# Optimization experiments

Hardware: AMD Instinct MI355X
Metric: run time of the kernel (lower is better)

The kernel has to match this reference:

```python
import jax, jax.numpy as jnp
import numpy as np

N = 100000      # nodes
E = 1_600_000   # edges (avg degree 16)
DIMS = [(64, 64), (64, 64), (64, 40)]  # gnn_layers [64,64,64,40]


def setup_inputs() -> dict:
    key = jax.random.key(0)
    ks = jax.random.split(key, 2 + 3 * len(DIMS))
    inp = {
        "x": jax.random.normal(ks[0], (N, DIMS[0][0]), jnp.float32),
        "edge_index": jax.random.randint(ks[1], (2, E), 0, N),
    }
    k = 2
    for i, (din, dout) in enumerate(DIMS):
        s = 1.0 / np.sqrt(din)
        inp[f"Wl{i}"] = jax.random.uniform(ks[k], (din, dout), jnp.float32, -s, s); k += 1
        inp[f"bl{i}"] = jax.random.uniform(ks[k], (dout,), jnp.float32, -s, s); k += 1
        inp[f"Wr{i}"] = jax.random.uniform(ks[k], (din, dout), jnp.float32, -s, s); k += 1
    return inp


def _sage_conv(x, src, dst, Wl, bl, Wr):
    # PyG SAGEConv (mean aggr): out = lin_l(mean_{j in N(i)} x_j) + lin_r(x_i)
    deg = jax.ops.segment_sum(jnp.ones((src.shape[0],), x.dtype), dst, num_segments=N)
    agg = jax.ops.segment_sum(x[src], dst, num_segments=N)  # [N, din] scatter-add
    agg = agg / jnp.clip(deg, 1.0)[:, None]                  # mean; isolated nodes -> 0
    return agg @ Wl + bl + x @ Wr


def reference(x, edge_index, Wl0, bl0, Wr0, Wl1, bl1, Wr1, Wl2, bl2, Wr2):
    src, dst = edge_index[0], edge_index[1]
    h = x
    params = [(Wl0, bl0, Wr0), (Wl1, bl1, Wr1), (Wl2, bl2, Wr2)]
    for i, (Wl, bl, Wr) in enumerate(params):
        h = _sage_conv(h, src, dst, Wl, bl, Wr)
        if i != len(params) - 1:
            h = jax.nn.relu(h)
            # F.dropout with training=False is identity (eval mode)
    return jax.nn.log_softmax(h, axis=1)
```

## Files before the change

### kernel.cpp

```cpp
#include <hip/hip_runtime.h>
#include <math.h>

#define ACT_RELU 0
#define ACT_LSM  1
#define BSH 8
#define MAXNB 512

typedef __attribute__((ext_vector_type(8))) short bf16x8;
typedef __attribute__((ext_vector_type(4))) float f32x4;

__device__ __forceinline__ unsigned f2bf(float f) {
  unsigned u = __float_as_uint(f);
  u += 0x7fffu + ((u >> 16) & 1u);
  return u >> 16;
}
__device__ __forceinline__ float bflo(unsigned u) { return __uint_as_float(u << 16); }
__device__ __forceinline__ float bfhi(unsigned u) { return __uint_as_float(u & 0xffff0000u); }

__global__ void k_histB(const int* __restrict__ dst, int* __restrict__ bucket_cnt,
                        int E, int NB) {
  __shared__ int cntL[MAXNB];
  int t = threadIdx.x;
  for (int b = t; b < NB; b += 256) cntL[b] = 0;
  __syncthreads();
  int e0 = blockIdx.x * 4096;
  int e1 = min(e0 + 4096, E);
  for (int i = e0 + t; i < e1; i += 256) atomicAdd(&cntL[dst[i] >> BSH], 1);
  __syncthreads();
  for (int b = t; b < NB; b += 256)
    if (cntL[b]) atomicAdd(&bucket_cnt[b], cntL[b]);
}

__global__ void k_bscan(const int* __restrict__ bucket_cnt, int* __restrict__ bucket_base,
                        int* __restrict__ bucket_cursor, int NB) {
  __shared__ int sm[MAXNB];
  int t = threadIdx.x;
  sm[t] = (t < NB) ? bucket_cnt[t] : 0;
  __syncthreads();
  for (int off = 1; off < MAXNB; off <<= 1) {
    int x = (t >= off) ? sm[t - off] : 0;
    __syncthreads();
    sm[t] += x;
    __syncthreads();
  }
  int ex = (t == 0) ? 0 : sm[t - 1];
  if (t <= NB) bucket_base[t] = ex;
  if (t < NB) bucket_cursor[t] = ex;
}

__global__ void k_partition(const int* __restrict__ src, const int* __restrict__ dst,
                            int* __restrict__ bucket_cursor, int2* __restrict__ tmp,
                            int E, int NB) {
  __shared__ int cntL[MAXNB];
  __shared__ int baseL[MAXNB];
  int t = threadIdx.x;
  for (int b = t; b < NB; b += 256) cntL[b] = 0;
  __syncthreads();
  int e0 = blockIdx.x * 4096;
  int e1 = min(e0 + 4096, E);
  for (int i = e0 + t; i < e1; i += 256) atomicAdd(&cntL[dst[i] >> BSH], 1);
  __syncthreads();
  for (int b = t; b < NB; b += 256) {
    int c = cntL[b];
    baseL[b] = c ? atomicAdd(&bucket_cursor[b], c) : 0;
    cntL[b] = 0;
  }
  __syncthreads();
  for (int i = e0 + t; i < e1; i += 256) {
    int s = src[i], d = dst[i];
    int b = d >> BSH;
    int r = atomicAdd(&cntL[b], 1);
    tmp[baseL[b] + r] = make_int2(s, d);
  }
}

__global__ void __launch_bounds__(256) k_bmake(const int2* __restrict__ tmp,
                                               const int* __restrict__ bucket_base,
                                               int* __restrict__ row_ptr,
                                               int* __restrict__ edge_src,
                                               int N, int E, int NB) {
  __shared__ int cntL[256];
  __shared__ int scanL[256];
  int b = blockIdx.x;
  int t = threadIdx.x;
  int e0 = bucket_base[b], e1 = bucket_base[b + 1];
  cntL[t] = 0;
  __syncthreads();
  for (int i = e0 + t; i < e1; i += 256) atomicAdd(&cntL[tmp[i].y & 255], 1);
  __syncthreads();
  int v = cntL[t];
  scanL[t] = v;
  __syncthreads();
  for (int off = 1; off < 256; off <<= 1) {
    int x = (t >= off) ? scanL[t - off] : 0;
    __syncthreads();
    scanL[t] += x;
    __syncthreads();
  }
  int exc = scanL[t] - v;
  int node = (b << BSH) + t;
  if (node < N) row_ptr[node] = e0 + exc;
  if (b == NB - 1 && t == 0) row_ptr[N] = E;
  __syncthreads();
  cntL[t] = e0 + exc;
  __syncthreads();
  for (int i = e0 + t; i < e1; i += 256) {
    int2 e = tmp[i];
    int p = atomicAdd(&cntL[e.y & 255], 1);
    edge_src[p] = e.x;
  }
}

__global__ void k_hist(const int* __restrict__ dst, int* __restrict__ cnt, int E) {
  int i = blockIdx.x * blockDim.x + threadIdx.x;
  if (i < E) atomicAdd(&cnt[dst[i]], 1);
}

__global__ void k_scan_part(const int* __restrict__ cnt, int* __restrict__ bsum, int M) {
  __shared__ int sm[256];
  int t = threadIdx.x;
  int base = blockIdx.x * 2048 + t * 8;
  int s = 0;
#pragma unroll
  for (int j = 0; j < 8; ++j) { int i = base + j; if (i < M) s += cnt[i]; }
  sm[t] = s;
  __syncthreads();
  for (int off = 128; off > 0; off >>= 1) {
    if (t < off) sm[t] += sm[t + off];
    __syncthreads();
  }
  if (t == 0) bsum[blockIdx.x] = sm[0];
}

__global__ void k_scan_mid(const int* __restrict__ bsum, int* __restrict__ boff, int nb) {
  int l = threadIdx.x;
  int v = (l < nb) ? bsum[l] : 0;
  int inc = v;
  for (int off = 1; off < 64; off <<= 1) {
    int u = __shfl_up(inc, off);
    if (l >= off) inc += u;
  }
  if (l < nb) boff[l] = inc - v;
}

__global__ void k_scan_final(const int* __restrict__ cnt, const int* __restrict__ boff,
                             int* __restrict__ row_ptr, int* __restrict__ cursor, int M) {
  __shared__ int sm[256];
  int t = threadIdx.x;
  int base = blockIdx.x * 2048 + t * 8;
  int v[8];
  int s = 0;
#pragma unroll
  for (int j = 0; j < 8; ++j) { int i = base + j; v[j] = (i < M) ? cnt[i] : 0; s += v[j]; }
  sm[t] = s;
  __syncthreads();
  for (int off = 1; off < 256; off <<= 1) {
    int x = (t >= off) ? sm[t - off] : 0;
    __syncthreads();
    sm[t] += x;
    __syncthreads();
  }
  int run = boff[blockIdx.x] + sm[t] - s;
#pragma unroll
  for (int j = 0; j < 8; ++j) {
    int i = base + j;
    if (i < M) { row_ptr[i] = run; cursor[i] = run; }
    run += v[j];
  }
}

__global__ void k_fill(const int* __restrict__ src, const int* __restrict__ dst,
                       int* __restrict__ cursor, int* __restrict__ edge_src, int E) {
  int i = blockIdx.x * blockDim.x + threadIdx.x;
  if (i < E) {
    int d = dst[i];
    int p = atomicAdd(&cursor[d], 1);
    edge_src[p] = src[i];
  }
}

__global__ void __launch_bounds__(256) k_cast(const float* __restrict__ x,
                                              unsigned short* __restrict__ xb, int n) {
  int i = blockIdx.x * 256 + threadIdx.x;
  if (i * 8 < n) {
    const float4* p = (const float4*)(x + (size_t)i * 8);
    float4 a = p[0], b = p[1];
    uint4 w;
    w.x = f2bf(a.x) | (f2bf(a.y) << 16);
    w.y = f2bf(a.z) | (f2bf(a.w) << 16);
    w.z = f2bf(b.x) | (f2bf(b.y) << 16);
    w.w = f2bf(b.z) | (f2bf(b.w) << 16);
    *(uint4*)(xb + (size_t)i * 8) = w;
  }
}

__global__ void __launch_bounds__(256) k_aggmean(const unsigned short* __restrict__ h,
                                                 const int* __restrict__ row_ptr,
                                                 const int* __restrict__ edge_src,
                                                 unsigned short* __restrict__ Mb, int n) {
  int t = threadIdx.x;
  int lane = t & 63;
  int g = lane & 7;
  int i = blockIdx.x * 32 + (t >> 6) * 8 + (lane >> 3);
  if (i >= n) return;
  int rp0 = row_ptr[i], rp1 = row_ptr[i + 1];
  int deg = rp1 - rp0;
  float a[8];
#pragma unroll
  for (int c = 0; c < 8; ++c) a[c] = 0.f;

  for (int base = 0; base < deg; base += 8) {
    int idx = rp0 + base + g;
    int sv = (idx < rp1) ? edge_src[idx] : 0;
    int cnt = min(8, deg - base);
    uint4 v0, v1, v2, v3, v4, v5, v6, v7;
#pragma unroll
    for (int e = 0; e < 8; ++e) {
      int s = __shfl(sv, (lane & ~7) | e);
      const uint4* p = (const uint4*)(h + (size_t)s * 64) + g;
      if (e == 0 && e < cnt) v0 = *p;
      if (e == 1 && e < cnt) v1 = *p;
      if (e == 2 && e < cnt) v2 = *p;
      if (e == 3 && e < cnt) v3 = *p;
      if (e == 4 && e < cnt) v4 = *p;
      if (e == 5 && e < cnt) v5 = *p;
      if (e == 6 && e < cnt) v6 = *p;
      if (e == 7 && e < cnt) v7 = *p;
    }
#define ACCUM(vv, ee)                                                   \
    if ((ee) < cnt) {                                                   \
      a[0] += bflo(vv.x); a[1] += bfhi(vv.x);                           \
      a[2] += bflo(vv.y); a[3] += bfhi(vv.y);                           \
      a[4] += bflo(vv.z); a[5] += bfhi(vv.z);                           \
      a[6] += bflo(vv.w); a[7] += bfhi(vv.w);                           \
    }
    ACCUM(v0, 0) ACCUM(v1, 1) ACCUM(v2, 2) ACCUM(v3, 3)
    ACCUM(v4, 4) ACCUM(v5, 5) ACCUM(v6, 6) ACCUM(v7, 7)
#undef ACCUM
  }

  float scale = (deg > 0) ? (1.0f / (float)deg) : 0.f;
  uint4 w;
  w.x = f2bf(a[0] * scale) | (f2bf(a[1] * scale) << 16);
  w.y = f2bf(a[2] * scale) | (f2bf(a[3] * scale) << 16);
  w.z = f2bf(a[4] * scale) | (f2bf(a[5] * scale) << 16);
  w.w = f2bf(a[6] * scale) | (f2bf(a[7] * scale) << 16);
  *((uint4*)(Mb + (size_t)i * 64) + g) = w;
}

template <int DOUT, int ACT>
__global__ void __launch_bounds__(256) k_gemm(const unsigned short* __restrict__ Ma,
                                              const unsigned short* __restrict__ Ha,
                                              const float* __restrict__ Wl,
                                              const float* __restrict__ Wr,
                                              const float* __restrict__ bias,
                                              void* __restrict__ outv, int n) {
  constexpr int NT = (DOUT + 15) / 16;
  constexpr int PADN = NT * 16;
  __shared__ unsigned short Wlds[128 * PADN];
  int t = threadIdx.x;
  for (int idx = t; idx < 128 * PADN; idx += 256) {
    int k = idx / PADN, nn = idx % PADN;
    float v = 0.f;
    if (nn < DOUT) v = (k < 64) ? Wl[k * DOUT + nn] : Wr[(k - 64) * DOUT + nn];
    int fi = ((((k >> 5) * NT + (nn >> 4)) * 16 + (nn & 15)) * 4 + ((k >> 3) & 3)) * 8 + (k & 7);
    Wlds[fi] = (unsigned short)f2bf(v);
  }
  __syncthreads();

  int lane = t & 63;
  int c = lane & 15;
  int kb = lane >> 4;

  bf16x8 bf[4][NT];
#pragma unroll
  for (int s = 0; s < 4; ++s)
#pragma unroll
    for (int nt = 0; nt < NT; ++nt)
      bf[s][nt] = *(const bf16x8*)&Wlds[(((s * NT + nt) * 16 + c) * 4 + kb) * 8];

  int r0 = (blockIdx.x * 4 + (t >> 6)) * 16;
  int row = r0 + c;
  if (row >= n) row = n - 1;
  size_t rb = (size_t)row * 64 + kb * 8;
  bf16x8 af[4];
  af[0] = *(const bf16x8*)(Ma + rb);
  af[1] = *(const bf16x8*)(Ma + rb + 32);
  af[2] = *(const bf16x8*)(Ha + rb);
  af[3] = *(const bf16x8*)(Ha + rb + 32);

  f32x4 acc[NT];
#pragma unroll
  for (int nt = 0; nt < NT; ++nt) acc[nt] = (f32x4){0.f, 0.f, 0.f, 0.f};
#pragma unroll
  for (int s = 0; s < 4; ++s)
#pragma unroll
    for (int nt = 0; nt < NT; ++nt)
      acc[nt] = __builtin_amdgcn_mfma_f32_16x16x32_bf16(af[s], bf[s][nt], acc[nt], 0, 0, 0);

  int rbase = r0 + kb * 4;
  if (ACT == ACT_RELU) {
    unsigned short* out = (unsigned short*)outv;
#pragma unroll
    for (int nt = 0; nt < NT; ++nt) {
      float bval = bias[nt * 16 + c];
#pragma unroll
      for (int r = 0; r < 4; ++r) {
        int R = rbase + r;
        if (R < n) {
          float v = fmaxf(acc[nt][r] + bval, 0.f);
          out[(size_t)R * DOUT + nt * 16 + c] = (unsigned short)f2bf(v);
        }
      }
    }
  } else {
    float* out = (float*)outv;
    float bv[NT];
#pragma unroll
    for (int nt = 0; nt < NT; ++nt) bv[nt] = ((nt * 16 + c) < DOUT) ? bias[nt * 16 + c] : 0.f;
#pragma unroll
    for (int r = 0; r < 4; ++r) {
      int R = rbase + r;
      float v[NT];
      float m = -INFINITY;
#pragma unroll
      for (int nt = 0; nt < NT; ++nt) {
        bool valid = (nt * 16 + c) < DOUT;
        v[nt] = valid ? (acc[nt][r] + bv[nt]) : -INFINITY;
        m = fmaxf(m, v[nt]);
      }
#pragma unroll
      for (int off = 1; off < 16; off <<= 1) m = fmaxf(m, __shfl_xor(m, off));
      float es = 0.f;
#pragma unroll
      for (int nt = 0; nt < NT; ++nt)
        if ((nt * 16 + c) < DOUT) es += expf(v[nt] - m);
#pragma unroll
      for (int off = 1; off < 16; off <<= 1) es += __shfl_xor(es, off);
      float lse = logf(es);
      if (R < n) {
#pragma unroll
        for (int nt = 0; nt < NT; ++nt)
          if ((nt * 16 + c) < DOUT) out[(size_t)R * DOUT + nt * 16 + c] = v[nt] - m - lse;
      }
    }
  }
}

extern "C" void kernel_launch(void* const* d_in, const int* in_sizes, int n_in,
                              void* d_out, int out_size, void* d_ws, size_t ws_size,
                              hipStream_t stream) {
  const float* x   = (const float*)d_in[0];
  const int*   ei  = (const int*)d_in[1];
  const float* Wl0 = (const float*)d_in[2];
  const float* bl0 = (const float*)d_in[3];
  const float* Wr0 = (const float*)d_in[4];
  const float* Wl1 = (const float*)d_in[5];
  const float* bl1 = (const float*)d_in[6];
  const float* Wr1 = (const float*)d_in[7];
  const float* Wl2 = (const float*)d_in[8];
  const float* bl2 = (const float*)d_in[9];
  const float* Wr2 = (const float*)d_in[10];
  float* out = (float*)d_out;

  int N = in_sizes[0] / 64;
  int E = in_sizes[1] / 2;
  int M = N + 1;
  int NB = (N + 255) >> BSH;
  const int* src = ei;
  const int* dst = ei + E;

  char* p = (char*)d_ws;
  auto alloc = [&](size_t bytes) {
    char* r = p;
    p += (bytes + 255) & ~(size_t)255;
    return r;
  };
  int* cnt      = (int*)alloc((size_t)M * 4);
  int* row_ptr  = (int*)alloc((size_t)M * 4);
  int* cursor   = (int*)alloc((size_t)M * 4);
  int* bsum     = (int*)alloc(256 * 4);
  int* boff     = (int*)alloc(256 * 4);
  int* bk_cnt   = (int*)alloc((MAXNB + 1) * 4);
  int* bk_base  = (int*)alloc((MAXNB + 1) * 4);
  int* bk_cur   = (int*)alloc((MAXNB + 1) * 4);
  int* edge_src = (int*)alloc((size_t)E * 4);
  size_t szR1 = (size_t)E * 8 > (size_t)N * 128 ? (size_t)E * 8 : (size_t)N * 128;
  char* R1              = alloc(szR1);
  unsigned short* Mb    = (unsigned short*)alloc((size_t)N * 128);
  unsigned short* hbA   = (unsigned short*)alloc((size_t)N * 128);
  if ((size_t)(p - (char*)d_ws) > ws_size) return;

  bool bucketed = (NB <= MAXNB);
  int eb4 = (E + 4095) / 4096;

  if (bucketed) {
    hipMemsetAsync(bk_cnt, 0, (MAXNB + 1) * 4, stream);
    k_histB<<<eb4, 256, 0, stream>>>(dst, bk_cnt, E, NB);
    k_bscan<<<1, MAXNB, 0, stream>>>(bk_cnt, bk_base, bk_cur, NB);
    k_partition<<<eb4, 256, 0, stream>>>(src, dst, bk_cur, (int2*)R1, E, NB);
    k_bmake<<<NB, 256, 0, stream>>>((const int2*)R1, bk_base, row_ptr, edge_src, N, E, NB);
  } else {
    hipMemsetAsync(cnt, 0, (size_t)M * 4, stream);
    k_hist<<<(E + 255) / 256, 256, 0, stream>>>(dst, cnt, E);
    int nb = (M + 2047) / 2048;
    k_scan_part<<<nb, 256, 0, stream>>>(cnt, bsum, M);
    k_scan_mid<<<1, 64, 0, stream>>>(bsum, boff, nb);
    k_scan_final<<<nb, 256, 0, stream>>>(cnt, boff, row_ptr, cursor, M);
    k_fill<<<(E + 255) / 256, 256, 0, stream>>>(src, dst, cursor, edge_src, E);
  }

  unsigned short* xb  = (unsigned short*)R1;
  unsigned short* hbB = (unsigned short*)R1;

  int cb = (N * 64 / 8 + 255) / 256;
  int ab = (N + 31) / 32;
  int gb = (N + 63) / 64;

  k_cast<<<cb, 256, 0, stream>>>(x, xb, N * 64);
  k_aggmean<<<ab, 256, 0, stream>>>(xb, row_ptr, edge_src, Mb, N);
  k_gemm<64, ACT_RELU><<<gb, 256, 0, stream>>>(Mb, xb, Wl0, Wr0, bl0, hbA, N);
  k_aggmean<<<ab, 256, 0, stream>>>(hbA, row_ptr, edge_src, Mb, N);
  k_gemm<64, ACT_RELU><<<gb, 256, 0, stream>>>(Mb, hbA, Wl1, Wr1, bl1, hbB, N);
  k_aggmean<<<ab, 256, 0, stream>>>(hbB, row_ptr, edge_src, Mb, N);
  k_gemm<40, ACT_LSM><<<gb, 256, 0, stream>>>(Mb, hbB, Wl2, Wr2, bl2, out, N);
}
```

Baseline: 217.4 us.

## Fuse mean aggregation into per-layer GEMM kernel via LDS staging

Merges the separate aggregation and GEMM kernels into one per-layer kernel. Each wave gathers neighbor features for its 16 rows, writes the bf16 means into LDS, and feeds them straight into the MFMA, so the intermediate mean buffer never goes to global memory and three launches are removed. Host memsets are replaced by a small zeroing kernel, and a separate buffer is allocated for the second hidden layer instead of aliasing R1. The cost is that each block now does the gather for 64 rows with a larger LDS footprint, which may lower occupancy and latency hiding during the irregular gather.

Measured after the change: 208.8 us. 1.04x faster.

```diff
diff --git a/kernel.cpp b/kernel.cpp
--- a/kernel.cpp
+++ b/kernel.cpp
@@ -16,6 +16,11 @@
 }
 __device__ __forceinline__ float bflo(unsigned u) { return __uint_as_float(u << 16); }
 __device__ __forceinline__ float bfhi(unsigned u) { return __uint_as_float(u & 0xffff0000u); }
+
+__global__ void k_zero(int* __restrict__ p, int n) {
+  int i = blockIdx.x * 256 + threadIdx.x;
+  if (i < n) p[i] = 0;
+}
 
 __global__ void k_histB(const int* __restrict__ dst, int* __restrict__ bucket_cnt,
                         int E, int NB) {
@@ -194,71 +199,20 @@
   }
 }
 
-__global__ void __launch_bounds__(256) k_aggmean(const unsigned short* __restrict__ h,
-                                                 const int* __restrict__ row_ptr,
-                                                 const int* __restrict__ edge_src,
-                                                 unsigned short* __restrict__ Mb, int n) {
-  int t = threadIdx.x;
-  int lane = t & 63;
-  int g = lane & 7;
-  int i = blockIdx.x * 32 + (t >> 6) * 8 + (lane >> 3);
-  if (i >= n) return;
-  int rp0 = row_ptr[i], rp1 = row_ptr[i + 1];
-  int deg = rp1 - rp0;
-  float a[8];
-#pragma unroll
-  for (int c = 0; c < 8; ++c) a[c] = 0.f;
-
-  for (int base = 0; base < deg; base += 8) {
-    int idx = rp0 + base + g;
-    int sv = (idx < rp1) ? edge_src[idx] : 0;
-    int cnt = min(8, deg - base);
-    uint4 v0, v1, v2, v3, v4, v5, v6, v7;
-#pragma unroll
-    for (int e = 0; e < 8; ++e) {
-      int s = __shfl(sv, (lane & ~7) | e);
-      const uint4* p = (const uint4*)(h + (size_t)s * 64) + g;
-      if (e == 0 && e < cnt) v0 = *p;
-      if (e == 1 && e < cnt) v1 = *p;
-      if (e == 2 && e < cnt) v2 = *p;
-      if (e == 3 && e < cnt) v3 = *p;
-      if (e == 4 && e < cnt) v4 = *p;
-      if (e == 5 && e < cnt) v5 = *p;
-      if (e == 6 && e < cnt) v6 = *p;
-      if (e == 7 && e < cnt) v7 = *p;
-    }
-#define ACCUM(vv, ee)                                                   \
-    if ((ee) < cnt) {                                                   \
-      a[0] += bflo(vv.x); a[1] += bfhi(vv.x);                           \
-      a[2] += bflo(vv.y); a[3] += bfhi(vv.y);                           \
-      a[4] += bflo(vv.z); a[5] += bfhi(vv.z);                           \
-      a[6] += bflo(vv.w); a[7] += bfhi(vv.w);                           \
-    }
-    ACCUM(v0, 0) ACCUM(v1, 1) ACCUM(v2, 2) ACCUM(v3, 3)
-    ACCUM(v4, 4) ACCUM(v5, 5) ACCUM(v6, 6) ACCUM(v7, 7)
-#undef ACCUM
-  }
-
-  float scale = (deg > 0) ? (1.0f / (float)deg) : 0.f;
-  uint4 w;
-  w.x = f2bf(a[0] * scale) | (f2bf(a[1] * scale) << 16);
-  w.y = f2bf(a[2] * scale) | (f2bf(a[3] * scale) << 16);
-  w.z = f2bf(a[4] * scale) | (f2bf(a[5] * scale) << 16);
-  w.w = f2bf(a[6] * scale) | (f2bf(a[7] * scale) << 16);
-  *((uint4*)(Mb + (size_t)i * 64) + g) = w;
-}
-
 template <int DOUT, int ACT>
-__global__ void __launch_bounds__(256) k_gemm(const unsigned short* __restrict__ Ma,
-                                              const unsigned short* __restrict__ Ha,
-                                              const float* __restrict__ Wl,
-                                              const float* __restrict__ Wr,
-                                              const float* __restrict__ bias,
-                                              void* __restrict__ outv, int n) {
+__global__ void __launch_bounds__(256) k_layer(const unsigned short* __restrict__ h,
+                                               const int* __restrict__ row_ptr,
+                                               const int* __restrict__ edge_src,
+                                               const float* __restrict__ Wl,
+                                               const float* __restrict__ Wr,
+                                               const float* __restrict__ bias,
+                                               void* __restrict__ outv, int n) {
   constexpr int NT = (DOUT + 15) / 16;
   constexpr int PADN = NT * 16;
   __shared__ unsigned short Wlds[128 * PADN];
-  int t = threadIdx.x;
+  __shared__ unsigned short meanL[4][16 * 72];
+  int t = threadIdx.x;
+
   for (int idx = t; idx < 128 * PADN; idx += 256) {
     int k = idx / PADN, nn = idx % PADN;
     float v = 0.f;
@@ -266,12 +220,63 @@
     int fi = ((((k >> 5) * NT + (nn >> 4)) * 16 + (nn & 15)) * 4 + ((k >> 3) & 3)) * 8 + (k & 7);
     Wlds[fi] = (unsigned short)f2bf(v);
   }
-  __syncthreads();
-
-  int lane = t & 63;
+
+  int w = t >> 6, lane = t & 63;
+  int r0 = (blockIdx.x * 4 + w) * 16;
+  int g = lane & 7;
+
+  for (int half = 0; half < 2; ++half) {
+    int node = half * 8 + (lane >> 3);
+    int i = r0 + node;
+    float a[8];
+#pragma unroll
+    for (int c = 0; c < 8; ++c) a[c] = 0.f;
+    float scale = 0.f;
+    if (i < n) {
+      int rp0 = row_ptr[i], rp1 = row_ptr[i + 1];
+      int deg = rp1 - rp0;
+      scale = (deg > 0) ? (1.0f / (float)deg) : 0.f;
+      for (int base = 0; base < deg; base += 8) {
+        int idx = rp0 + base + g;
+        int sv = (idx < rp1) ? edge_src[idx] : 0;
+        int cnt = min(8, deg - base);
+        uint4 v0, v1, v2, v3, v4, v5, v6, v7;
+#pragma unroll
+        for (int e = 0; e < 8; ++e) {
+          int s = __shfl(sv, (lane & ~7) | e);
+          const uint4* p = (const uint4*)(h + (size_t)s * 64) + g;
+          if (e == 0 && e < cnt) v0 = *p;
+          if (e == 1 && e < cnt) v1 = *p;
+          if (e == 2 && e < cnt) v2 = *p;
+          if (e == 3 && e < cnt) v3 = *p;
+          if (e == 4 && e < cnt) v4 = *p;
+          if (e == 5 && e < cnt) v5 = *p;
+          if (e == 6 && e < cnt) v6 = *p;
+          if (e == 7 && e < cnt) v7 = *p;
+        }
+#define ACCUM(vv, ee)                                                   \
+        if ((ee) < cnt) {                                               \
+          a[0] += bflo(vv.x); a[1] += bfhi(vv.x);                       \
+          a[2] += bflo(vv.y); a[3] += bfhi(vv.y);                       \
+          a[4] += bflo(vv.z); a[5] += bfhi(vv.z);                       \
+          a[6] += bflo(vv.w); a[7] += bfhi(vv.w);                       \
+        }
+        ACCUM(v0, 0) ACCUM(v1, 1) ACCUM(v2, 2) ACCUM(v3, 3)
+        ACCUM(v4, 4) ACCUM(v5, 5) ACCUM(v6, 6) ACCUM(v7, 7)
+#undef ACCUM
+      }
+    }
+    uint4 wv;
+    wv.x = f2bf(a[0] * scale) | (f2bf(a[1] * scale) << 16);
+    wv.y = f2bf(a[2] * scale) | (f2bf(a[3] * scale) << 16);
+    wv.z = f2bf(a[4] * scale) | (f2bf(a[5] * scale) << 16);
+    wv.w = f2bf(a[6] * scale) | (f2bf(a[7] * scale) << 16);
+    *(uint4*)&meanL[w][node * 72 + g * 8] = wv;
+  }
+  __syncthreads();
+
   int c = lane & 15;
   int kb = lane >> 4;
-
   bf16x8 bf[4][NT];
 #pragma unroll
   for (int s = 0; s < 4; ++s)
@@ -279,15 +284,14 @@
     for (int nt = 0; nt < NT; ++nt)
       bf[s][nt] = *(const bf16x8*)&Wlds[(((s * NT + nt) * 16 + c) * 4 + kb) * 8];
 
-  int r0 = (blockIdx.x * 4 + (t >> 6)) * 16;
+  bf16x8 af[4];
+  af[0] = *(const bf16x8*)&meanL[w][c * 72 + kb * 8];
+  af[1] = *(const bf16x8*)&meanL[w][c * 72 + 32 + kb * 8];
   int row = r0 + c;
   if (row >= n) row = n - 1;
   size_t rb = (size_t)row * 64 + kb * 8;
-  bf16x8 af[4];
-  af[0] = *(const bf16x8*)(Ma + rb);
-  af[1] = *(const bf16x8*)(Ma + rb + 32);
-  af[2] = *(const bf16x8*)(Ha + rb);
-  af[3] = *(const bf16x8*)(Ha + rb + 32);
+  af[2] = *(const bf16x8*)(h + rb);
+  af[3] = *(const bf16x8*)(h + rb + 32);
 
   f32x4 acc[NT];
 #pragma unroll
@@ -386,22 +390,22 @@
   int* bk_cur   = (int*)alloc((MAXNB + 1) * 4);
   int* edge_src = (int*)alloc((size_t)E * 4);
   size_t szR1 = (size_t)E * 8 > (size_t)N * 128 ? (size_t)E * 8 : (size_t)N * 128;
-  char* R1              = alloc(szR1);
-  unsigned short* Mb    = (unsigned short*)alloc((size_t)N * 128);
-  unsigned short* hbA   = (unsigned short*)alloc((size_t)N * 128);
+  char* R1            = alloc(szR1);
+  unsigned short* hbA = (unsigned short*)alloc((size_t)N * 128);
+  unsigned short* hbB = (unsigned short*)alloc((size_t)N * 128);
   if ((size_t)(p - (char*)d_ws) > ws_size) return;
 
   bool bucketed = (NB <= MAXNB);
   int eb4 = (E + 4095) / 4096;
 
   if (bucketed) {
-    hipMemsetAsync(bk_cnt, 0, (MAXNB + 1) * 4, stream);
+    k_zero<<<(MAXNB + 256) / 256, 256, 0, stream>>>(bk_cnt, MAXNB + 1);
     k_histB<<<eb4, 256, 0, stream>>>(dst, bk_cnt, E, NB);
     k_bscan<<<1, MAXNB, 0, stream>>>(bk_cnt, bk_base, bk_cur, NB);
     k_partition<<<eb4, 256, 0, stream>>>(src, dst, bk_cur, (int2*)R1, E, NB);
     k_bmake<<<NB, 256, 0, stream>>>((const int2*)R1, bk_base, row_ptr, edge_src, N, E, NB);
   } else {
-    hipMemsetAsync(cnt, 0, (size_t)M * 4, stream);
+    k_zero<<<(M + 255) / 256, 256, 0, stream>>>(cnt, M);
     k_hist<<<(E + 255) / 256, 256, 0, stream>>>(dst, cnt, E);
     int nb = (M + 2047) / 2048;
     k_scan_part<<<nb, 256, 0, stream>>>(cnt, bsum, M);
@@ -410,18 +414,13 @@
     k_fill<<<(E + 255) / 256, 256, 0, stream>>>(src, dst, cursor, edge_src, E);
   }
 
-  unsigned short* xb  = (unsigned short*)R1;
-  unsigned short* hbB = (unsigned short*)R1;
+  unsigned short* xb = (unsigned short*)R1;
 
   int cb = (N * 64 / 8 + 255) / 256;
-  int ab = (N + 31) / 32;
   int gb = (N + 63) / 64;
 
   k_cast<<<cb, 256, 0, stream>>>(x, xb, N * 64);
-  k_aggmean<<<ab, 256, 0, stream>>>(xb, row_ptr, edge_src, Mb, N);
-  k_gemm<64, ACT_RELU><<<gb, 256, 0, stream>>>(Mb, xb, Wl0, Wr0, bl0, hbA, N);
-  k_aggmean<<<ab, 256, 0, stream>>>(hbA, row_ptr, edge_src, Mb, N);
-  k_gemm<64, ACT_RELU><<<gb, 256, 0, stream>>>(Mb, hbA, Wl1, Wr1, bl1, hbB, N);
-  k_aggmean<<<ab, 256, 0, stream>>>(hbB, row_ptr, edge_src, Mb, N);
-  k_gemm<40, ACT_LSM><<<gb, 256, 0, stream>>>(Mb, hbB, Wl2, Wr2, bl2, out, N);
-}
+  k_layer<64, ACT_RELU><<<gb, 256, 0, stream>>>(xb, row_ptr, edge_src, Wl0, Wr0, bl0, hbA, N);
+  k_layer<64, ACT_RELU><<<gb, 256, 0, stream>>>(hbA, row_ptr, edge_src, Wl1, Wr1, bl1, hbB, N);
+  k_layer<40, ACT_LSM><<<gb, 256, 0, stream>>>(hbB, row_ptr, edge_src, Wl2, Wr2, bl2, out, N);
+}
```
